# Kernel optimization log

Hardware: AMD Instinct MI355X
Metric: run time of the kernel (lower is better)

Reference implementation:

```python
import jax, jax.numpy as jnp
import numpy as np

SWITCH_W = 30.0
TOL = 5
DECAY = 0.7
FP_PEN = 10.0
INV_PEN = 100.0
CLASS_W = jnp.array([1.0, 1.0, SWITCH_W, SWITCH_W], dtype=jnp.float32)


def setup_inputs() -> dict:
    key = jax.random.key(0)
    k1, k2, k3 = jax.random.split(key, 3)
    B, S, C = 512, 8192, 4
    logits = jax.random.normal(k1, (B, S, C), dtype=jnp.float32)
    labels = jax.random.randint(k2, (B, S), 0, 4, dtype=jnp.int32)
    # sprinkle ignore_index (-100) positions like real padded sequences
    drop = jax.random.uniform(k3, (B, S)) < 0.05
    labels = jnp.where(drop, jnp.int32(-100), labels)
    return {"logits": logits, "labels": labels}


def _mode_multiplier(labels, preds):
    """Sequential state machine over time; carry = (pred_mode, true_mode) per batch row."""
    B, S = labels.shape

    def step(carry, xs):
        pm, tm = carry
        lab, pred = xs  # [B] each
        valid = lab != -100
        # invalid transition penalty on predicted switches
        bad = ((pred == 2) & (pm == 0)) | ((pred == 3) & (pm == 1))
        pen = jnp.where(valid & bad, INV_PEN, 1.0)
        new_pm = jnp.where(valid, jnp.where((pred == 0) | (pred == 2), 0, 1), pm)
        # reward correct mode switches (true label agrees with pred switch)
        good = ((lab == 2) & (tm == 1) & (pred == 2)) | ((lab == 3) & (tm == 0) & (pred == 3))
        bonus = jnp.where(valid & good, 0.1, 1.0)
        new_tm = jnp.where(valid & ((lab == 0) | (lab == 2)), 0,
                           jnp.where(valid & ((lab == 1) | (lab == 3)), 1, tm))
        return (new_pm, new_tm), pen * bonus

    init = (jnp.zeros((B,), jnp.int32), jnp.zeros((B,), jnp.int32))
    _, mult = jax.lax.scan(step, init, (labels.T, preds.T))
    return mult.T  # [B, S]


def _nearest_dist(mask):
    """For each position, distance to nearest True in the same row; BIG if none."""
    B, S = mask.shape
    BIG = jnp.int32(S + TOL + 2)

    def f(c, m):
        c = jnp.where(m, jnp.int32(0), jnp.minimum(c + 1, BIG))
        return c, c

    init = jnp.full((B,), BIG, jnp.int32)
    _, fwd = jax.lax.scan(f, init, mask.T)
    _, bwd = jax.lax.scan(f, init, mask[:, ::-1].T)
    return jnp.minimum(fwd.T, bwd.T[:, ::-1])


def _loss(logits, labels):
    preds = jnp.argmax(logits, axis=-1).astype(jnp.int32)
    valid = labels != -100
    labs = jnp.where(valid, labels, 0)
    logp = jax.nn.log_softmax(logits, axis=-1)
    ce = -jnp.take_along_axis(logp, labs[..., None], axis=-1)[..., 0] * CLASS_W[labs]

    mult = _mode_multiplier(labels, preds)
    for c in (2, 3):
        true_m = labels == c
        pred_m = preds == c
        d_true = _nearest_dist(true_m)
        d_pred = _nearest_dist(pred_m)
        has_true = true_m.any(axis=1, keepdims=True)
        has_pred = pred_m.any(axis=1, keepdims=True)
        # multipliers at predicted-switch positions
        mp = jnp.where(
            pred_m,
            jnp.where(
                has_true,
                jnp.where(d_true == 0, 0.1,
                          jnp.where(d_true <= TOL, DECAY ** d_true.astype(jnp.float32), FP_PEN)),
                FP_PEN * 2.0),
            1.0)
        # multipliers at true-switch positions
        mt = jnp.where(
            true_m,
            jnp.where(has_pred, jnp.where(d_pred > TOL, 2.0, 1.0), 3.0),
            1.0)
        mult = mult * mp * mt

    vf = valid.astype(ce.dtype)
    total = (ce * mult * vf).sum()
    return total / jnp.maximum(vf.sum(), 1.0)


def reference(logits, labels):
    return _loss(logits, labels)
```

## Files before the change

### kernel.cpp

```cpp
#include <hip/hip_runtime.h>
#include <math.h>

#define BROWS 512
#define SLEN  8192
#define NT    1024
#define CHUNK 8
#define NWRD  (SLEN / 32)
#define MWRD  (NWRD + 2)

__device__ __forceinline__ int win_dist(const unsigned int* __restrict__ M, int t) {
    int sI = t + 27;
    int w  = sI >> 5;
    int off = sI & 31;
    unsigned long long val =
        ((unsigned long long)M[w] | ((unsigned long long)M[w + 1] << 32)) >> off;
    unsigned int win = (unsigned int)val & 0x7FFu;
    if (win & 32u) return 0;
    unsigned int dn = win & 31u;
    unsigned int up = (win >> 6) & 31u;
    int d = 99;
    if (dn) d = 5 - (31 - __clz((int)dn));
    if (up) { int du = __ffs((int)up); if (du < d) d = du; }
    return d;
}

__device__ __forceinline__ float decay_pow(int d) {
    return (d == 1) ? 0.7f : (d == 2) ? 0.49f : (d == 3) ? 0.343f
         : (d == 4) ? 0.2401f : 0.16807f;
}

#define P1(i, v, lab, cev) {                                                  \
    float m01 = fmaxf((v).x, (v).y), m23 = fmaxf((v).z, (v).w);               \
    float best = fmaxf(m01, m23);                                             \
    int pred = (best == (v).x) ? 0 : (best == (v).y) ? 1                      \
             : (best == (v).z) ? 2 : 3;                                       \
    bool valid = ((lab) != -100);                                             \
    cnt += valid ? 1 : 0;                                                     \
    int l = valid ? ((lab) & 3) : 0;                                          \
    float se = __expf((v).x - best) + __expf((v).y - best) +                  \
               __expf((v).z - best) + __expf((v).w - best);                   \
    float lse = best + __logf(se);                                            \
    float xl = (l == 0) ? (v).x : (l == 1) ? (v).y : (l == 2) ? (v).z : (v).w;\
    float wc = (l >= 2) ? 30.0f : 1.0f;                                       \
    cev = valid ? (lse - xl) * wc : 0.0f;                                     \
    pkw |= (unsigned long long)(unsigned)(pred | (l << 2) | (valid ? 16 : 0)) \
           << (8 * (i));                                                      \
    if (pred == 2) mp2 |= 1u << (i);                                          \
    if (pred == 3) mp3 |= 1u << (i);                                          \
    if (valid && l == 2) mt2 |= 1u << (i);                                    \
    if (valid && l == 3) mt3 |= 1u << (i);                                    \
    if (valid) summary = 4u | (unsigned)(pred & 1) | ((unsigned)(l & 1) << 1);\
}

#define P3(i, cev) {                                                          \
    int t = base + (i);                                                       \
    unsigned int pk = (unsigned int)(pkw >> (8 * (i))) & 31u;                 \
    int pred = pk & 3, l = (pk >> 2) & 3;                                     \
    bool valid = (pk & 16) != 0;                                              \
    float m = 1.0f;                                                           \
    if (valid) {                                                              \
        bool bad = (pred == 2 && pm == 0) || (pred == 3 && pm == 1);          \
        if (bad) m *= 100.0f;                                                 \
        bool good = (l == 2 && tm == 1 && pred == 2) ||                       \
                    (l == 3 && tm == 0 && pred == 3);                         \
        if (good) m *= 0.1f;                                                  \
        pm = pred & 1;                                                        \
        tm = l & 1;                                                           \
    }                                                                         \
    if (pred >= 2) {                                                          \
        bool has = (pred == 2) ? hasT2 : hasT3;                               \
        if (!has) m *= 20.0f;                                                 \
        else {                                                                \
            int d = win_dist(s_m[(pred - 2) << 1], t);                        \
            m *= (d == 0) ? 0.1f : (d <= 5) ? decay_pow(d) : 10.0f;           \
        }                                                                     \
    }                                                                         \
    if (valid && l >= 2) {                                                    \
        bool has = (l == 2) ? hasP2 : hasP3;                                  \
        if (!has) m *= 3.0f;                                                  \
        else if (win_dist(s_m[1 + ((l - 2) << 1)], t) > 5) m *= 2.0f;         \
    }                                                                         \
    acc += (cev) * m;                                                         \
}

__global__ __launch_bounds__(NT, 4) void row_loss_kernel(
    const float* __restrict__ logits, const int* __restrict__ labels,
    double* __restrict__ psum, unsigned int* __restrict__ pcnt)
{
    __shared__ unsigned int  s_m[4][MWRD];
    __shared__ unsigned int  s_wave[16];
    __shared__ unsigned int  s_flags;
    __shared__ double        s_red[16];
    __shared__ int           s_redc[16];

    const int row  = blockIdx.x;
    const int tid  = threadIdx.x;
    const int lane = tid & 63;
    const int wid  = tid >> 6;
    const int base = tid * CHUNK;

    if (tid < 4) { s_m[tid][0] = 0u; s_m[tid][MWRD - 1] = 0u; }
    if (tid == 4) s_flags = 0u;

    const float4* lg4 = (const float4*)logits + (size_t)row * SLEN + base;
    const int4*   lb4 = (const int4*)(labels + (size_t)row * SLEN + base);

    int4 la0 = lb4[0], la1 = lb4[1];
    float4 q0 = lg4[0], q1 = lg4[1], q2 = lg4[2], q3 = lg4[3];
    float4 q4 = lg4[4], q5 = lg4[5], q6 = lg4[6], q7 = lg4[7];

    unsigned long long pkw = 0ull;
    unsigned int mt2 = 0, mp2 = 0, mt3 = 0, mp3 = 0;
    unsigned int summary = 0;
    int cnt = 0;
    float ce0, ce1, ce2, ce3, ce4, ce5, ce6, ce7;

    P1(0, q0, la0.x, ce0); P1(1, q1, la0.y, ce1);
    P1(2, q2, la0.z, ce2); P1(3, q3, la0.w, ce3);
    P1(4, q4, la1.x, ce4); P1(5, q5, la1.y, ce5);
    P1(6, q6, la1.z, ce6); P1(7, q7, la1.w, ce7);

    {
        int sh = (tid & 3) * 8;
        unsigned int w0 = mt2 << sh, w1 = mp2 << sh, w2 = mt3 << sh, w3 = mp3 << sh;
        w0 |= __shfl_xor(w0, 1); w0 |= __shfl_xor(w0, 2);
        w1 |= __shfl_xor(w1, 1); w1 |= __shfl_xor(w1, 2);
        w2 |= __shfl_xor(w2, 1); w2 |= __shfl_xor(w2, 2);
        w3 |= __shfl_xor(w3, 1); w3 |= __shfl_xor(w3, 2);
        if ((tid & 3) == 0) {
            int wi = 1 + (tid >> 2);
            s_m[0][wi] = w0; s_m[1][wi] = w1; s_m[2][wi] = w2; s_m[3][wi] = w3;
        }
    }
    {
        unsigned int fl = (mt2 ? 1u : 0u) | (mp2 ? 2u : 0u) |
                          (mt3 ? 4u : 0u) | (mp3 ? 8u : 0u);
        #pragma unroll
        for (int s = 32; s > 0; s >>= 1) fl |= __shfl_xor(fl, s);
        if (lane == 0 && fl) atomicOr(&s_flags, fl);
    }

    unsigned int inc = summary;
    #pragma unroll
    for (int st = 1; st < 64; st <<= 1) {
        unsigned int o = __shfl_up(inc, st);
        if (lane >= st && !(inc & 4u)) inc = o;
    }
    unsigned int exc = __shfl_up(inc, 1);
    if (lane == 0) exc = 0u;
    if (lane == 63) s_wave[wid] = inc;
    __syncthreads();

    unsigned int wv = (lane < 16) ? s_wave[lane] : 0u;
    #pragma unroll
    for (int st = 1; st < 16; st <<= 1) {
        unsigned int o = __shfl_up(wv, st);
        if (lane >= st && !(wv & 4u)) wv = o;
    }
    unsigned int wpre = __shfl(wv, (wid > 0) ? (wid - 1) : 0);
    if (wid == 0) wpre = 0u;

    unsigned int pre = (exc & 4u) ? exc : wpre;
    int pm = (int)(pre & 1u), tm = (int)((pre >> 1) & 1u);
    const unsigned int flags = s_flags;
    const bool hasT2 = flags & 1u, hasP2 = flags & 2u;
    const bool hasT3 = flags & 4u, hasP3 = flags & 8u;

    float acc = 0.0f;
    P3(0, ce0); P3(1, ce1); P3(2, ce2); P3(3, ce3);
    P3(4, ce4); P3(5, ce5); P3(6, ce6); P3(7, ce7);

    double dacc = (double)acc;
    #pragma unroll
    for (int o = 32; o > 0; o >>= 1) {
        dacc += __shfl_down(dacc, o);
        cnt  += __shfl_down(cnt, o);
    }
    if (lane == 0) { s_red[wid] = dacc; s_redc[wid] = cnt; }
    __syncthreads();
    if (tid == 0) {
        double tot = 0.0; unsigned int c = 0;
        #pragma unroll
        for (int i = 0; i < 16; ++i) { tot += s_red[i]; c += (unsigned int)s_redc[i]; }
        psum[row] = tot;
        pcnt[row] = c;
    }
}

__global__ __launch_bounds__(512) void finalize_kernel(
    const double* __restrict__ psum, const unsigned int* __restrict__ pcnt,
    float* __restrict__ out)
{
    __shared__ double       sd[8];
    __shared__ unsigned int sc[8];
    int tid = threadIdx.x, lane = tid & 63, wid = tid >> 6;
    double v = psum[tid];
    unsigned int c = pcnt[tid];
    #pragma unroll
    for (int o = 32; o > 0; o >>= 1) {
        v += __shfl_down(v, o);
        c += __shfl_down(c, o);
    }
    if (lane == 0) { sd[wid] = v; sc[wid] = c; }
    __syncthreads();
    if (tid == 0) {
        double t = 0.0; unsigned int cc = 0;
        #pragma unroll
        for (int i = 0; i < 8; ++i) { t += sd[i]; cc += sc[i]; }
        double d = (cc > 0u) ? (double)cc : 1.0;
        out[0] = (float)(t / d);
    }
}

extern "C" void kernel_launch(void* const* d_in, const int* in_sizes, int n_in,
                              void* d_out, int out_size, void* d_ws, size_t ws_size,
                              hipStream_t stream) {
    const float* logits = (const float*)d_in[0];
    const int*   labels = (const int*)d_in[1];
    float* out = (float*)d_out;
    double* psum = (double*)d_ws;
    unsigned int* pcnt = (unsigned int*)(psum + BROWS);

    row_loss_kernel<<<BROWS, NT, 0, stream>>>(logits, labels, psum, pcnt);
    finalize_kernel<<<1, 512, 0, stream>>>(psum, pcnt, out);
}
```

Measured before the change: 121.7 us.

## Switch to strided element mapping with ballot bitmasks and lookback mode state

```diff
diff --git a/kernel.cpp b/kernel.cpp
--- a/kernel.cpp
+++ b/kernel.cpp
@@ -4,7 +4,6 @@
 #define BROWS 512
 #define SLEN  8192
 #define NT    1024
-#define CHUNK 8
 #define NWRD  (SLEN / 32)
 #define MWRD  (NWRD + 2)
 
@@ -29,43 +28,78 @@
          : (d == 4) ? 0.2401f : 0.16807f;
 }
 
-#define P1(i, v, lab, cev) {                                                  \
-    float m01 = fmaxf((v).x, (v).y), m23 = fmaxf((v).z, (v).w);               \
+#define STEP(k, qv, lab, cev) {                                               \
+    float m01 = fmaxf((qv).x, (qv).y), m23 = fmaxf((qv).z, (qv).w);           \
     float best = fmaxf(m01, m23);                                             \
-    int pred = (best == (v).x) ? 0 : (best == (v).y) ? 1                      \
-             : (best == (v).z) ? 2 : 3;                                       \
+    int pred = (best == (qv).x) ? 0 : (best == (qv).y) ? 1                    \
+             : (best == (qv).z) ? 2 : 3;                                      \
     bool valid = ((lab) != -100);                                             \
-    cnt += valid ? 1 : 0;                                                     \
     int l = valid ? ((lab) & 3) : 0;                                          \
-    float se = __expf((v).x - best) + __expf((v).y - best) +                  \
-               __expf((v).z - best) + __expf((v).w - best);                   \
+    float se = __expf((qv).x - best) + __expf((qv).y - best) +                \
+               __expf((qv).z - best) + __expf((qv).w - best);                 \
     float lse = best + __logf(se);                                            \
-    float xl = (l == 0) ? (v).x : (l == 1) ? (v).y : (l == 2) ? (v).z : (v).w;\
-    float wc = (l >= 2) ? 30.0f : 1.0f;                                       \
-    cev = valid ? (lse - xl) * wc : 0.0f;                                     \
+    float xl = (l == 0) ? (qv).x : (l == 1) ? (qv).y                          \
+             : (l == 2) ? (qv).z : (qv).w;                                    \
+    cev = valid ? (lse - xl) * ((l >= 2) ? 30.0f : 1.0f) : 0.0f;              \
     pkw |= (unsigned long long)(unsigned)(pred | (l << 2) | (valid ? 16 : 0)) \
-           << (8 * (i));                                                      \
-    if (pred == 2) mp2 |= 1u << (i);                                          \
-    if (pred == 3) mp3 |= 1u << (i);                                          \
-    if (valid && l == 2) mt2 |= 1u << (i);                                    \
-    if (valid && l == 3) mt3 |= 1u << (i);                                    \
-    if (valid) summary = 4u | (unsigned)(pred & 1) | ((unsigned)(l & 1) << 1);\
-}
-
-#define P3(i, cev) {                                                          \
-    int t = base + (i);                                                       \
-    unsigned int pk = (unsigned int)(pkw >> (8 * (i))) & 31u;                 \
+           << (8 * (k));                                                      \
+    unsigned long long bT2 = __ballot(valid && l == 2);                       \
+    unsigned long long bP2 = __ballot(pred == 2);                             \
+    unsigned long long bT3 = __ballot(valid && l == 3);                       \
+    unsigned long long bP3 = __ballot(pred == 3);                             \
+    unsigned long long bV  = __ballot(valid);                                 \
+    unsigned long long bPM = __ballot(valid && (pred & 1));                   \
+    unsigned long long bTM = __ballot(valid && (l & 1));                      \
+    int wk = (k) * 32 + wid * 2;                                              \
+    if (lane == 0) {                                                          \
+        s_m[0][1 + wk] = (unsigned)bT2; s_m[1][1 + wk] = (unsigned)bP2;       \
+        s_m[2][1 + wk] = (unsigned)bT3; s_m[3][1 + wk] = (unsigned)bP3;       \
+        s_v[wk] = (unsigned)bV; s_pm[wk] = (unsigned)bPM;                     \
+        s_tm[wk] = (unsigned)bTM;                                             \
+    } else if (lane == 32) {                                                  \
+        s_m[0][2 + wk] = (unsigned)(bT2 >> 32);                               \
+        s_m[1][2 + wk] = (unsigned)(bP2 >> 32);                               \
+        s_m[2][2 + wk] = (unsigned)(bT3 >> 32);                               \
+        s_m[3][2 + wk] = (unsigned)(bP3 >> 32);                               \
+        s_v[wk + 1] = (unsigned)(bV >> 32);                                   \
+        s_pm[wk + 1] = (unsigned)(bPM >> 32);                                 \
+        s_tm[wk + 1] = (unsigned)(bTM >> 32);                                 \
+    }                                                                         \
+    fl |= (bT2 ? 1u : 0u) | (bP2 ? 2u : 0u) | (bT3 ? 4u : 0u)                 \
+        | (bP3 ? 8u : 0u);                                                    \
+    cntw += (int)__popcll(bV);                                                \
+}
+
+#define P3(k, cev) {                                                          \
+    int t = (k) * NT + tid;                                                   \
+    unsigned pk = (unsigned)(pkw >> (8 * (k))) & 31u;                         \
     int pred = pk & 3, l = (pk >> 2) & 3;                                     \
     bool valid = (pk & 16) != 0;                                              \
     float m = 1.0f;                                                           \
-    if (valid) {                                                              \
+    if (valid && (pred >= 2 || l >= 2)) {                                     \
+        int w = t >> 5, b = t & 31;                                           \
+        unsigned hi = s_v[w];                                                 \
+        unsigned lo = (w > 0) ? s_v[w - 1] : 0u;                              \
+        unsigned long long x = (((unsigned long long)hi) << 32) | lo;         \
+        x &= (1ull << (b + 32)) - 1ull;                                       \
+        int pm = 0, tm = 0;                                                   \
+        if (x) {                                                              \
+            int p = 63 - __clzll(x);                                          \
+            int ww = w - 1 + (p >> 5); int pb = p & 31;                       \
+            pm = (int)((s_pm[ww] >> pb) & 1u);                                \
+            tm = (int)((s_tm[ww] >> pb) & 1u);                                \
+        } else if (w >= 2) {               \
+            int ww = w - 2; unsigned xx = 0u;                                 \
+            while (ww >= 0 && (xx = s_v[ww]) == 0u) --ww;                     \
+            if (ww >= 0) { int pb = 31 - __clz((int)xx);                      \
+                pm = (int)((s_pm[ww] >> pb) & 1u);                            \
+                tm = (int)((s_tm[ww] >> pb) & 1u); }                          \
+        }                                                                     \
         bool bad = (pred == 2 && pm == 0) || (pred == 3 && pm == 1);          \
         if (bad) m *= 100.0f;                                                 \
         bool good = (l == 2 && tm == 1 && pred == 2) ||                       \
                     (l == 3 && tm == 0 && pred == 3);                         \
         if (good) m *= 0.1f;                                                  \
-        pm = pred & 1;                                                        \
-        tm = l & 1;                                                           \
     }                                                                         \
     if (pred >= 2) {                                                          \
         bool has = (pred == 2) ? hasT2 : hasT3;                               \
@@ -87,82 +121,50 @@
     const float* __restrict__ logits, const int* __restrict__ labels,
     double* __restrict__ psum, unsigned int* __restrict__ pcnt)
 {
-    __shared__ unsigned int  s_m[4][MWRD];
-    __shared__ unsigned int  s_wave[16];
-    __shared__ unsigned int  s_flags;
-    __shared__ double        s_red[16];
-    __shared__ int           s_redc[16];
+    __shared__ unsigned int s_m[4][MWRD];
+    __shared__ unsigned int s_v[NWRD];
+    __shared__ unsigned int s_pm[NWRD];
+    __shared__ unsigned int s_tm[NWRD];
+    __shared__ unsigned int s_wfl[16];
+    __shared__ double       s_red[16];
+    __shared__ int          s_redc[16];
 
     const int row  = blockIdx.x;
     const int tid  = threadIdx.x;
     const int lane = tid & 63;
     const int wid  = tid >> 6;
-    const int base = tid * CHUNK;
 
     if (tid < 4) { s_m[tid][0] = 0u; s_m[tid][MWRD - 1] = 0u; }
-    if (tid == 4) s_flags = 0u;
-
-    const float4* lg4 = (const float4*)logits + (size_t)row * SLEN + base;
-    const int4*   lb4 = (const int4*)(labels + (size_t)row * SLEN + base);
-
-    int4 la0 = lb4[0], la1 = lb4[1];
-    float4 q0 = lg4[0], q1 = lg4[1], q2 = lg4[2], q3 = lg4[3];
-    float4 q4 = lg4[4], q5 = lg4[5], q6 = lg4[6], q7 = lg4[7];
+
+    const float4* lg4 = (const float4*)logits + (size_t)row * SLEN;
+    const int*    lb  = labels + (size_t)row * SLEN;
+
+    float4 q0 = lg4[0 * NT + tid], q1 = lg4[1 * NT + tid];
+    float4 q2 = lg4[2 * NT + tid], q3 = lg4[3 * NT + tid];
+    float4 q4 = lg4[4 * NT + tid], q5 = lg4[5 * NT + tid];
+    float4 q6 = lg4[6 * NT + tid], q7 = lg4[7 * NT + tid];
+    int la0 = lb[0 * NT + tid], la1 = lb[1 * NT + tid];
+    int la2 = lb[2 * NT + tid], la3 = lb[3 * NT + tid];
+    int la4 = lb[4 * NT + tid], la5 = lb[5 * NT + tid];
+    int la6 = lb[6 * NT + tid], la7 = lb[7 * NT + tid];
 
     unsigned long long pkw = 0ull;
-    unsigned int mt2 = 0, mp2 = 0, mt3 = 0, mp3 = 0;
-    unsigned int summary = 0;
-    int cnt = 0;
+    unsigned int fl = 0u;
+    int cntw = 0;
     float ce0, ce1, ce2, ce3, ce4, ce5, ce6, ce7;
 
-    P1(0, q0, la0.x, ce0); P1(1, q1, la0.y, ce1);
-    P1(2, q2, la0.z, ce2); P1(3, q3, la0.w, ce3);
-    P1(4, q4, la1.x, ce4); P1(5, q5, la1.y, ce5);
-    P1(6, q6, la1.z, ce6); P1(7, q7, la1.w, ce7);
-
-    {
-        int sh = (tid & 3) * 8;
-        unsigned int w0 = mt2 << sh, w1 = mp2 << sh, w2 = mt3 << sh, w3 = mp3 << sh;
-        w0 |= __shfl_xor(w0, 1); w0 |= __shfl_xor(w0, 2);
-        w1 |= __shfl_xor(w1, 1); w1 |= __shfl_xor(w1, 2);
-        w2 |= __shfl_xor(w2, 1); w2 |= __shfl_xor(w2, 2);
-        w3 |= __shfl_xor(w3, 1); w3 |= __shfl_xor(w3, 2);
-        if ((tid & 3) == 0) {
-            int wi = 1 + (tid >> 2);
-            s_m[0][wi] = w0; s_m[1][wi] = w1; s_m[2][wi] = w2; s_m[3][wi] = w3;
-        }
-    }
-    {
-        unsigned int fl = (mt2 ? 1u : 0u) | (mp2 ? 2u : 0u) |
-                          (mt3 ? 4u : 0u) | (mp3 ? 8u : 0u);
-        #pragma unroll
-        for (int s = 32; s > 0; s >>= 1) fl |= __shfl_xor(fl, s);
-        if (lane == 0 && fl) atomicOr(&s_flags, fl);
-    }
-
-    unsigned int inc = summary;
-    #pragma unroll
-    for (int st = 1; st < 64; st <<= 1) {
-        unsigned int o = __shfl_up(inc, st);
-        if (lane >= st && !(inc & 4u)) inc = o;
-    }
-    unsigned int exc = __shfl_up(inc, 1);
-    if (lane == 0) exc = 0u;
-    if (lane == 63) s_wave[wid] = inc;
+    STEP(0, q0, la0, ce0); STEP(1, q1, la1, ce1);
+    STEP(2, q2, la2, ce2); STEP(3, q3, la3, ce3);
+    STEP(4, q4, la4, ce4); STEP(5, q5, la5, ce5);
+    STEP(6, q6, la6, ce6); STEP(7, q7, la7, ce7);
+
+    if (lane == 0) s_wfl[wid] = fl;
     __syncthreads();
 
-    unsigned int wv = (lane < 16) ? s_wave[lane] : 0u;
-    #pragma unroll
-    for (int st = 1; st < 16; st <<= 1) {
-        unsigned int o = __shfl_up(wv, st);
-        if (lane >= st && !(wv & 4u)) wv = o;
-    }
-    unsigned int wpre = __shfl(wv, (wid > 0) ? (wid - 1) : 0);
-    if (wid == 0) wpre = 0u;
-
-    unsigned int pre = (exc & 4u) ? exc : wpre;
-    int pm = (int)(pre & 1u), tm = (int)((pre >> 1) & 1u);
-    const unsigned int flags = s_flags;
+    uint4 f0 = *(const uint4*)(s_wfl + 0), f1 = *(const uint4*)(s_wfl + 4);
+    uint4 f2 = *(const uint4*)(s_wfl + 8), f3 = *(const uint4*)(s_wfl + 12);
+    unsigned int flags = f0.x | f0.y | f0.z | f0.w | f1.x | f1.y | f1.z | f1.w
+                       | f2.x | f2.y | f2.z | f2.w | f3.x | f3.y | f3.z | f3.w;
     const bool hasT2 = flags & 1u, hasP2 = flags & 2u;
     const bool hasT3 = flags & 4u, hasP3 = flags & 8u;
 
@@ -172,11 +174,8 @@
 
     double dacc = (double)acc;
     #pragma unroll
-    for (int o = 32; o > 0; o >>= 1) {
-        dacc += __shfl_down(dacc, o);
-        cnt  += __shfl_down(cnt, o);
-    }
-    if (lane == 0) { s_red[wid] = dacc; s_redc[wid] = cnt; }
+    for (int o = 32; o > 0; o >>= 1) dacc += __shfl_down(dacc, o);
+    if (lane == 0) { s_red[wid] = dacc; s_redc[wid] = cntw; }
     __syncthreads();
     if (tid == 0) {
         double tot = 0.0; unsigned int c = 0;
```

After: 127.0 us. 4.4% more time.
